# Kernel tuning notes

Hardware: AMD Instinct MI355X
Metric: run time of the kernel (lower is better)

## Reference

```python
import jax, jax.numpy as jnp
import numpy as np

FEAT = 128
N_RBF = 20
CUTOFF = 5.0
NUM_CONV = 3
N_ATOMS = 8000
N_EDGES = 160000
N_MOLS = 100
EPS = 1e-15


def silu(x):
    return x * jax.nn.sigmoid(x)


def setup_inputs() -> dict:
    key = jax.random.key(0)
    ks = jax.random.split(key, 16)
    F = FEAT

    def w(k, shape, fan_in):
        return jax.random.normal(k, shape, dtype=jnp.float32) / np.sqrt(fan_in).astype(np.float32)

    nbr0 = jax.random.randint(ks[12], (N_EDGES,), 0, N_ATOMS)
    # avoid self-edges (would give zero distance)
    nbr1 = (nbr0 + 1 + jax.random.randint(ks[13], (N_EDGES,), 0, N_ATOMS - 1)) % N_ATOMS
    return {
        "xyz": jax.random.uniform(ks[0], (N_ATOMS, 3), dtype=jnp.float32) * 10.0,
        "emb_table": jax.random.normal(ks[1], (100, F), dtype=jnp.float32),
        "msg_w1": w(ks[2], (NUM_CONV, F, F), F),
        "msg_b1": jnp.zeros((NUM_CONV, F), jnp.float32),
        "msg_w2": w(ks[3], (NUM_CONV, F, 3 * F), F),
        "msg_b2": jnp.zeros((NUM_CONV, 3 * F), jnp.float32),
        "rbf_w": w(ks[4], (NUM_CONV, N_RBF, 3 * F), N_RBF),
        "rbf_b": jnp.zeros((NUM_CONV, 3 * F), jnp.float32),
        "upd_u": w(ks[5], (NUM_CONV, F, F), F),
        "upd_v": w(ks[6], (NUM_CONV, F, F), F),
        "upd_w1": w(ks[7], (NUM_CONV, 2 * F, F), 2 * F),
        "upd_b1": jnp.zeros((NUM_CONV, F), jnp.float32),
        "upd_w2": w(ks[8], (NUM_CONV, F, 3 * F), F),
        "upd_b2": jnp.zeros((NUM_CONV, 3 * F), jnp.float32),
        "ro_w1": w(ks[9], (F, F // 2), F),
        "ro_b1": jnp.zeros((F // 2,), jnp.float32),
        "ro_w2": w(ks[10], (F // 2, 1), F // 2),
        "ro_b2": jnp.zeros((1,), jnp.float32),
        "z": jax.random.randint(ks[11], (N_ATOMS,), 0, 100),
        "nbrs": jnp.stack([nbr0, nbr1], axis=1),
        "mol_idx": jnp.sort(jax.random.randint(ks[14], (N_ATOMS,), 0, N_MOLS)),
    }


def painn_forward(xyz, emb_table, msg_w1, msg_b1, msg_w2, msg_b2, rbf_w, rbf_b,
                  upd_u, upd_v, upd_w1, upd_b1, upd_w2, upd_b2,
                  ro_w1, ro_b1, ro_w2, ro_b2, z, nbrs, mol_idx):
    F = FEAT
    N = xyz.shape[0]
    # r_ij points from nbrs[:,0] (center i) to nbrs[:,1] (neighbor j)
    r_ij = xyz[nbrs[:, 1]] - xyz[nbrs[:, 0]]            # (E, 3)
    d = jnp.sqrt(jnp.sum(r_ij * r_ij, axis=-1))         # (E,)
    unit = r_ij / d[:, None]                            # (E, 3)
    # PaiNN sinc radial basis: sin(n*pi*d/cutoff)/d, n = 1..n_rbf
    n = jnp.arange(1, N_RBF + 1, dtype=jnp.float32)
    rbf = jnp.sin(n[None, :] * jnp.pi * d[:, None] / CUTOFF) / d[:, None]  # (E, n_rbf)
    # cosine cutoff envelope
    env = jnp.where(d <= CUTOFF, 0.5 * (jnp.cos(jnp.pi * d / CUTOFF) + 1.0), 0.0)

    s = emb_table[z]                                    # (N, F)
    v = jnp.zeros((N, F, 3), dtype=s.dtype)             # (N, F, 3)

    for i in range(NUM_CONV):
        # ---- message block ----
        phi = silu(s @ msg_w1[i] + msg_b1[i]) @ msg_w2[i] + msg_b2[i]   # (N, 3F)
        w_s = (rbf @ rbf_w[i] + rbf_b[i]) * env[:, None]                # (E, 3F)
        inv = (phi[nbrs[:, 1]] * w_s).reshape(-1, 3, F)                 # (E, 3, F)
        split0 = inv[:, 0, :][..., None]                                # (E, F, 1)
        split1 = inv[:, 1, :]                                           # (E, F)
        split2 = inv[:, 2, :][..., None]                                # (E, F, 1)
        dv_ij = split2 * unit[:, None, :] + split0 * v[nbrs[:, 1]]      # (E, F, 3)
        ds = jax.ops.segment_sum(split1, nbrs[:, 0], num_segments=N)
        dv = jax.ops.segment_sum(dv_ij, nbrs[:, 0], num_segments=N)
        s = s + ds
        v = v + dv
        # ---- update block ----
        u_v = jnp.einsum('nfd,fg->ngd', v, upd_u[i])                    # (N, F, 3)
        v_v = jnp.einsum('nfd,fg->ngd', v, upd_v[i])                    # (N, F, 3)
        v_v_norm = jnp.sqrt(jnp.sum(v_v * v_v, axis=-1) + EPS)          # (N, F)
        stack = jnp.concatenate([s, v_v_norm], axis=-1)                 # (N, 2F)
        a = (silu(stack @ upd_w1[i] + upd_b1[i]) @ upd_w2[i] + upd_b2[i]).reshape(-1, 3, F)
        a_vv = a[:, 0, :][..., None]
        a_sv = a[:, 1, :]
        a_ss = a[:, 2, :]
        dv_u = u_v * a_vv
        ds_u = jnp.sum(u_v * v_v, axis=-1) * a_sv + a_ss
        s = s + ds_u
        v = v + dv_u

    # readout MLP + per-molecule sum pool (SumPool)
    atom_e = silu(s @ ro_w1 + ro_b1) @ ro_w2 + ro_b2                    # (N, 1)
    energy = jax.ops.segment_sum(atom_e, mol_idx, num_segments=N_MOLS)  # (N_MOLS, 1)
    return energy


def reference(xyz, emb_table, msg_w1, msg_b1, msg_w2, msg_b2, rbf_w, rbf_b,
              upd_u, upd_v, upd_w1, upd_b1, upd_w2, upd_b2,
              ro_w1, ro_b1, ro_w2, ro_b2, z, nbrs, mol_idx):
    return painn_forward(xyz, emb_table, msg_w1, msg_b1, msg_w2, msg_b2, rbf_w, rbf_b,
                         upd_u, upd_v, upd_w1, upd_b1, upd_w2, upd_b2,
                         ro_w1, ro_b1, ro_w2, ro_b2, z, nbrs, mol_idx)
```

## Files before the change

### kernel.cpp

```cpp
#include <hip/hip_runtime.h>

static constexpr int F = 128;
static constexpr int N_RBF = 20;
static constexpr int N_ATOMS = 8000;
static constexpr int NP = 8064;
static constexpr int N_EDGES = 160000;
static constexpr int N_MOLS = 100;
static constexpr float CUTOFF = 5.0f;
static constexpr size_t NFC = (size_t)NP * F;
static constexpr int REC = 28;
static constexpr int NPHI_BLK = NP / 32;
static constexpr int NBUILD_BLK = (N_EDGES + 255) / 256;
#define PIF 3.14159265358979323846f

typedef __attribute__((ext_vector_type(8))) short bf16x8;
typedef __attribute__((ext_vector_type(4))) float f32x4;
typedef unsigned short ushort_t;
typedef unsigned int uint_t;

__device__ __forceinline__ float silu_f(float x) { return x / (1.f + __expf(-x)); }

__device__ __forceinline__ ushort_t f2bf(float x) {
    union { float f; uint_t u; } v; v.f = x;
    uint_t r = v.u + 0x7fffu + ((v.u >> 16) & 1u);
// ... 220 lines not shown
                acc[i][j] = __builtin_amdgcn_mfma_f32_16x16x32_bf16(ahf[i], bhf[j], acc[i][j], 0, 0, 0);
                acc[i][j] = __builtin_amdgcn_mfma_f32_16x16x32_bf16(ahf[i], blf[j], acc[i][j], 0, 0, 0);
                acc[i][j] = __builtin_amdgcn_mfma_f32_16x16x32_bf16(alf[i], bhf[j], acc[i][j], 0, 0, 0);
            }
        if (it + 1 < 4) { writeA((it + 1) & 1); writeB((it + 1) & 1); }
        __syncthreads();
    }
    #pragma unroll
    for (int j = 0; j < 2; ++j) {
        int col = wn + j * 16 + row_l;
        float bval = b1[col];
        #pragma unroll
        for (int i = 0; i < 2; ++i)
            #pragma unroll
            for (int r = 0; r < 4; ++r) {
                int row = i * 16 + quad * 4 + r;
                float v = silu_f(acc[i][j][r] + bval);
                ushort_t h = f2bf(v);
                Hh[row * 136 + col] = h;
                Hl[row * 136 + col] = f2bf(v - bf2f(h));
            }
    }

    #pragma unroll
    for (int i = 0; i < 2; ++i)
        #pragma unroll
        for (int j = 0; j < 2; ++j)
            #pragma unroll
            for (int r = 0; r < 4; ++r) acc[i][j][r] = 0.f;
    loadB2(0); writeB(0);
    __syncthreads();
    #pragma unroll
    for (int it = 0; it < 12; ++it) {
        const int k0 = (it & 3) * 32;
        if (it + 1 < 12) loadB2(it + 1);
        bf16x8 ahf[2], alf[2], bhf[2], blf[2];
        #pragma unroll
        for (int i = 0; i < 2; ++i) {
            int ar = (i * 16 + row_l) * 136 + k0 + quad * 8;
            ahf[i] = *(const bf16x8*)&Hh[ar];
            alf[i] = *(const bf16x8*)&Hl[ar];
        }
        #pragma unroll
        for (int j = 0; j < 2; ++j) {
            int br = (wn + j * 16 + row_l) * 40 + quad * 8;
            bhf[j] = *(const bf16x8*)&Bh[it & 1][br];
            blf[j] = *(const bf16x8*)&Bl[it & 1][br];
        }
        #pragma unroll
        for (int i = 0; i < 2; ++i)
            #pragma unroll
            for (int j = 0; j < 2; ++j) {
                acc[i][j] = __builtin_amdgcn_mfma_f32_16x16x32_bf16(ahf[i], bhf[j], acc[i][j], 0, 0, 0);
                acc[i][j] = __builtin_amdgcn_mfma_f32_16x16x32_bf16(ahf[i], blf[j], acc[i][j], 0, 0, 0);
                acc[i][j] = __builtin_amdgcn_mfma_f32_16x16x32_bf16(alf[i], bhf[j], acc[i][j], 0, 0, 0);
            }
        if ((it & 3) == 3) {
            const int ct = it >> 2;
            #pragma unroll
            for (int j = 0; j < 2; ++j) {
                int col = ct * 128 + wn + j * 16 + row_l;
                float bval = b2[col];
                #pragma unroll
                for (int i = 0; i < 2; ++i)
                    #pragma unroll
                    for (int r = 0; r < 4; ++r) {
                        int row = i * 16 + quad * 4 + r;
                        C[(size_t)(m0 + row) * 384 + col] = acc[i][j][r] + bval;
                    }
            }
            #pragma unroll
            for (int i = 0; i < 2; ++i)
                #pragma unroll
                for (int j = 0; j < 2; ++j)
                    #pragma unroll
                    for (int r = 0; r < 4; ++r) acc[i][j][r] = 0.f;
        }
        if (it + 1 < 12) writeB((it + 1) & 1);
        __syncthreads();
    }
}

template<int TAIL>
__global__ __launch_bounds__(256) void updphi_kernel(
    float* __restrict__ s_io, float* __restrict__ v_io,
    const ushort_t* __restrict__ UVh, const ushort_t* __restrict__ UVl,
    const ushort_t* __restrict__ W1h, const ushort_t* __restrict__ W1l,
    const float* __restrict__ b1,
    const ushort_t* __restrict__ W2h, const ushort_t* __restrict__ W2l,
    const float* __restrict__ b2,
    const ushort_t* __restrict__ XW1h, const ushort_t* __restrict__ XW1l,
    const float* __restrict__ xb1,
    const ushort_t* __restrict__ XW2h, const ushort_t* __restrict__ XW2l,
    const float* __restrict__ xb2,
    float* __restrict__ phi_out,
    const float* __restrict__ w2ro, const float* __restrict__ b2ro,
    const int* __restrict__ mol, float* __restrict__ outp)
{
    __shared__ float uvv[96][260];
    __shared__ __align__(16) ushort_t Bh[2][128 * 40];
    __shared__ __align__(16) ushort_t Bl[2][128 * 40];
    __shared__ __align__(16) unsigned char AH[17408];
    __shared__ float molacc[128];
    __shared__ float redl[32][4];
    const int tid = threadIdx.x;
    const int wave = tid >> 6, lane = tid & 63;
    const int row_l = lane & 15, quad = lane >> 4;
    const int wn = wave * 32;
    const int m0 = blockIdx.x * 32;
    const int lrA = tid >> 3;
    const int ksA = (tid & 7) * 4;
    const int lrB = tid >> 1, ksB = (tid & 1) * 16;

    float* sS = &uvv[0][0];
    constexpr int SSTR = 132;

    {
        ushort_t* A0h = (ushort_t*)AH;
        ushort_t* A0l = A0h + 96 * 40;
        ushort_t* B0h = &Bh[0][0];
        ushort_t* B0l = &Bl[0][0];
        f32x4 acc0[6][4];
        #pragma unroll
        for (int i = 0; i < 6; ++i)
            #pragma unroll
            for (int j = 0; j < 4; ++j)
                #pragma unroll
                for (int r = 0; r < 4; ++r) acc0[i][j][r] = 0.f;
        for (int k0 = 0; k0 < 128; k0 += 32) {
            #pragma unroll
            for (int g = 0; g < 3; ++g) {
                int row = g * 32 + lrA;
                float4 v = *(const float4*)&v_io[(size_t)(m0 * 3 + row) * 128 + k0 + ksA];
                float e[4] = {v.x, v.y, v.z, v.w};
                ushort_t ph[4], pl[4];
                #pragma unroll
                for (int t = 0; t < 4; ++t) {
                    ushort_t h = f2bf(e[t]);
                    ph[t] = h; pl[t] = f2bf(e[t] - bf2f(h));
                }
                *(uint2*)&A0h[row * 40 + ksA] = *(uint2*)ph;
                *(uint2*)&A0l[row * 40 + ksA] = *(uint2*)pl;
            }
            {
                const ushort_t* bh = &UVh[(size_t)tid * 128 + k0];
                const ushort_t* bl = &UVl[(size_t)tid * 128 + k0];
                *(uint4*)&B0h[tid * 40 + 0]  = *(const uint4*)(bh + 0);
                *(uint4*)&B0h[tid * 40 + 8]  = *(const uint4*)(bh + 8);
                *(uint4*)&B0h[tid * 40 + 16] = *(const uint4*)(bh + 16);
                *(uint4*)&B0h[tid * 40 + 24] = *(const uint4*)(bh + 24);
                *(uint4*)&B0l[tid * 40 + 0]  = *(const uint4*)(bl + 0);
                *(uint4*)&B0l[tid * 40 + 8]  = *(const uint4*)(bl + 8);
                *(uint4*)&B0l[tid * 40 + 16] = *(const uint4*)(bl + 16);
                *(uint4*)&B0l[tid * 40 + 24] = *(const uint4*)(bl + 24);
            }
            __syncthreads();
            bf16x8 a0h[6], a0l[6], b0h[4], b0l[4];
            #pragma unroll
            for (int i = 0; i < 6; ++i) {
                int ar = (i * 16 + row_l) * 40 + quad * 8;
                a0h[i] = *(const bf16x8*)&A0h[ar];
                a0l[i] = *(const bf16x8*)&A0l[ar];
            }
            #pragma unroll
            for (int j = 0; j < 4; ++j) {
                int br = (wave * 64 + j * 16 + row_l) * 40 + quad * 8;
                b0h[j] = *(const bf16x8*)&B0h[br];
                b0l[j] = *(const bf16x8*)&B0l[br];
            }
            #pragma unroll
            for (int i = 0; i < 6; ++i)
                #pragma unroll
                for (int j = 0; j < 4; ++j) {
                    acc0[i][j] = __builtin_amdgcn_mfma_f32_16x16x32_bf16(a0h[i], b0h[j], acc0[i][j], 0, 0, 0);
                    acc0[i][j] = __builtin_amdgcn_mfma_f32_16x16x32_bf16(a0h[i], b0l[j], acc0[i][j], 0, 0, 0);
                    acc0[i][j] = __builtin_amdgcn_mfma_f32_16x16x32_bf16(a0l[i], b0h[j], acc0[i][j], 0, 0, 0);
                }
            __syncthreads();
        }
        #pragma unroll
        for (int i = 0; i < 6; ++i)
            #pragma unroll
            for (int j = 0; j < 4; ++j)
                #pragma unroll
                for (int r = 0; r < 4; ++r)
                    uvv[i * 16 + quad * 4 + r][wave * 64 + j * 16 + row_l] = acc0[i][j][r];
        __syncthreads();
    }

    ushort_t* Ah1 = (ushort_t*)AH;
    ushort_t* Al1 = Ah1 + 2 * 32 * 40;
    ushort_t* Hh  = (ushort_t*)AH;
    ushort_t* Hl  = Hh + 32 * 136;

    float4 rx;
    uint4 b_h0, b_h1, b_l0, b_l1;

    auto loadB1 = [&](int k0) {
        const ushort_t* bh = &W1h[(size_t)lrB * 256 + k0 + ksB];
        const ushort_t* bl = &W1l[(size_t)lrB * 256 + k0 + ksB];
        b_h0 = *(const uint4*)bh; b_h1 = *(const uint4*)(bh + 8);
        b_l0 = *(const uint4*)bl; b_l1 = *(const uint4*)(bl + 8);
    };
    auto writeB = [&](int buf) {
        *(uint4*)&Bh[buf][lrB * 40 + ksB]     = b_h0;
        *(uint4*)&Bh[buf][lrB * 40 + ksB + 8] = b_h1;
        *(uint4*)&Bl[buf][lrB * 40 + ksB]     = b_l0;
        *(uint4*)&Bl[buf][lrB * 40 + ksB + 8] = b_l1;
    };
    auto writeA1 = [&](int buf, int k0) {
        float e[4];
        if (k0 < 128) {
            e[0] = rx.x; e[1] = rx.y; e[2] = rx.z; e[3] = rx.w;
        } else {
            int f = k0 + ksA;
            #pragma unroll
            for (int t = 0; t < 4; ++t) {
                float x = uvv[lrA * 3 + 0][f + t];
                float y = uvv[lrA * 3 + 1][f + t];
                float z = uvv[lrA * 3 + 2][f + t];
                e[t] = sqrtf(x * x + y * y + z * z + 1e-15f);
            }
        }
        ushort_t ph[4], pl[4];
        #pragma unroll
        for (int t = 0; t < 4; ++t) {
            ushort_t h = f2bf(e[t]);
            ph[t] = h; pl[t] = f2bf(e[t] - bf2f(h));
        }
        *(uint2*)&Ah1[buf * 1280 + lrA * 40 + ksA] = *(uint2*)ph;
        *(uint2*)&Al1[buf * 1280 + lrA * 40 + ksA] = *(uint2*)pl;
    };

    f32x4 acc[2][2];
    #pragma unroll
    for (int i = 0; i < 2; ++i)
        #pragma unroll
        for (int j = 0; j < 2; ++j)
            #pragma unroll
            for (int r = 0; r < 4; ++r) acc[i][j][r] = 0.f;

    rx = *(const float4*)&s_io[(size_t)(m0 + lrA) * 128 + ksA];
    loadB1(0);
    writeA1(0, 0); writeB(0);
    __syncthreads();
    #pragma unroll
    for (int it = 0; it < 8; ++it) {
        const int k0n = (it + 1) * 32;
        if (it + 1 < 8) {
            if (k0n < 128) rx = *(const float4*)&s_io[(size_t)(m0 + lrA) * 128 + k0n + ksA];
            loadB1(k0n);
        }
        bf16x8 ahf[2], alf[2], bhf[2], blf[2];
        #pragma unroll
        for (int i = 0; i < 2; ++i) {
            int ar = (it & 1) * 1280 + (i * 16 + row_l) * 40 + quad * 8;
            ahf[i] = *(const bf16x8*)&Ah1[ar];
            alf[i] = *(const bf16x8*)&Al1[ar];
        }
        #pragma unroll
        for (int j = 0; j < 2; ++j) {
            int br = (wn + j * 16 + row_l) * 40 + quad * 8;
            bhf[j] = *(const bf16x8*)&Bh[it & 1][br];
            blf[j] = *(const bf16x8*)&Bl[it & 1][br];
        }
        #pragma unroll
        for (int i = 0; i < 2; ++i)
            #pragma unroll
            for (int j = 0; j < 2; ++j) {
                acc[i][j] = __builtin_amdgcn_mfma_f32_16x16x32_bf16(ahf[i], bhf[j], acc[i][j], 0, 0, 0);
                acc[i][j] = __builtin_amdgcn_mfma_f32_16x16x32_bf16(ahf[i], blf[j], acc[i][j], 0, 0, 0);
                acc[i][j] = __builtin_amdgcn_mfma_f32_16x16x32_bf16(alf[i], bhf[j], acc[i][j], 0, 0, 0);
            }
        if (it + 1 < 8) { writeA1((it + 1) & 1, k0n); writeB((it + 1) & 1); }
        __syncthreads();
    }
    #pragma unroll
    for (int j = 0; j < 2; ++j) {
        int col = wn + j * 16 + row_l;
        float bval = b1[col];
        #pragma unroll
        for (int i = 0; i < 2; ++i)
            #pragma unroll
            for (int r = 0; r < 4; ++r) {
                int row = i * 16 + quad * 4 + r;
                float v = silu_f(acc[i][j][r] + bval);
                ushort_t h = f2bf(v);
                Hh[row * 136 + col] = h;
                Hl[row * 136 + col] = f2bf(v - bf2f(h));
            }
    }

    constexpr int CT0 = TAIL ? 1 : 0;
    constexpr int NIT2 = (3 - CT0) * 4;
    auto loadB2 = [&](int it2) {
        int ct = CT0 + (it2 >> 2), k0 = (it2 & 3) * 32;
        const ushort_t* bh = &W2h[(size_t)(ct * 128 + lrB) * 128 + k0 + ksB];
        const ushort_t* bl = &W2l[(size_t)(ct * 128 + lrB) * 128 + k0 + ksB];
        b_h0 = *(const uint4*)bh; b_h1 = *(const uint4*)(bh + 8);
        b_l0 = *(const uint4*)bl; b_l1 = *(const uint4*)(bl + 8);
    };

    #pragma unroll
    for (int i = 0; i < 2; ++i)
        #pragma unroll
        for (int j = 0; j < 2; ++j)
            #pragma unroll
            for (int r = 0; r < 4; ++r) acc[i][j][r] = 0.f;
    f32x4 ssum[2][2];

    loadB2(0); writeB(0);
    __syncthreads();
    #pragma unroll
    for (int it = 0; it < NIT2; ++it) {
        const int k0 = (it & 3) * 32;
        if (it + 1 < NIT2) loadB2(it + 1);
        bf16x8 ahf[2], alf[2], bhf[2], blf[2];
        #pragma unroll
        for (int i = 0; i < 2; ++i) {
            int ar = (i * 16 + row_l) * 136 + k0 + quad * 8;
            ahf[i] = *(const bf16x8*)&Hh[ar];
            alf[i] = *(const bf16x8*)&Hl[ar];
        }
        #pragma unroll
        for (int j = 0; j < 2; ++j) {
            int br = (wn + j * 16 + row_l) * 40 + quad * 8;
            bhf[j] = *(const bf16x8*)&Bh[it & 1][br];
            blf[j] = *(const bf16x8*)&Bl[it & 1][br];
        }
        #pragma unroll
        for (int i = 0; i < 2; ++i)
            #pragma unroll
            for (int j = 0; j < 2; ++j) {
                acc[i][j] = __builtin_amdgcn_mfma_f32_16x16x32_bf16(ahf[i], bhf[j], acc[i][j], 0, 0, 0);
                acc[i][j] = __builtin_amdgcn_mfma_f32_16x16x32_bf16(ahf[i], blf[j], acc[i][j], 0, 0, 0);
                acc[i][j] = __builtin_amdgcn_mfma_f32_16x16x32_bf16(alf[i], bhf[j], acc[i][j], 0, 0, 0);
            }
        if ((it & 3) == 3) {
            const int ct = CT0 + (it >> 2);
            #pragma unroll
            for (int j = 0; j < 2; ++j) {
                int f = wn + j * 16 + row_l;
                float bval = b2[ct * 128 + f];
                #pragma unroll
                for (int i = 0; i < 2; ++i)
                    #pragma unroll
                    for (int r = 0; r < 4; ++r) {
                        int ln = i * 16 + quad * 4 + r;
                        float a = acc[i][j][r] + bval;
                        if (ct == 0) {
                            size_t vb = (size_t)(m0 + ln) * 3 * F + f;
                            v_io[vb]         += uvv[ln * 3 + 0][f] * a;
                            v_io[vb + F]     += uvv[ln * 3 + 1][f] * a;
                            v_io[vb + 2 * F] += uvv[ln * 3 + 2][f] * a;
                        } else if (ct == 1) {
                            float dot = uvv[ln * 3 + 0][f] * uvv[ln * 3 + 0][128 + f]
                                      + uvv[ln * 3 + 1][f] * uvv[ln * 3 + 1][128 + f]
                                      + uvv[ln * 3 + 2][f] * uvv[ln * 3 + 2][128 + f];
                            ssum[i][j][r] = dot * a;
                        } else {
                            float sv = s_io[(size_t)(m0 + ln) * F + f] + ssum[i][j][r] + a;
                            if constexpr (TAIL == 0) s_io[(size_t)(m0 + ln) * F + f] = sv;
                            sS[ln * SSTR + f] = sv;
                        }
                    }
            }
            #pragma unroll
            for (int i = 0; i < 2; ++i)
                #pragma unroll
                for (int j = 0; j < 2; ++j)
                    #pragma unroll
                    for (int r = 0; r < 4; ++r) acc[i][j][r] = 0.f;
        }
        if (it + 1 < NIT2) writeB((it + 1) & 1);
        __syncthreads();
    }

    if constexpr (TAIL == 1) { if (tid < 128) molacc[tid] = 0.f; }
    ushort_t* Ah3 = (ushort_t*)AH;
    ushort_t* Al3 = Ah3 + 2 * 1280;

    auto loadB31 = [&](int k0) {
        const ushort_t* bh = &XW1h[(size_t)lrB * 128 + k0 + ksB];
        const ushort_t* bl = &XW1l[(size_t)lrB * 128 + k0 + ksB];
        b_h0 = *(const uint4*)bh; b_h1 = *(const uint4*)(bh + 8);
        b_l0 = *(const uint4*)bl; b_l1 = *(const uint4*)(bl + 8);
    };
    auto writeA3 = [&](int buf, int k0) {
        float e[4];
        #pragma unroll
        for (int t = 0; t < 4; ++t) e[t] = sS[lrA * SSTR + k0 + ksA + t];
        ushort_t ph[4], pl[4];
        #pragma unroll
        for (int t = 0; t < 4; ++t) {
            ushort_t h = f2bf(e[t]);
            ph[t] = h; pl[t] = f2bf(e[t] - bf2f(h));
        }
        *(uint2*)&Ah3[buf * 1280 + lrA * 40 + ksA] = *(uint2*)ph;
        *(uint2*)&Al3[buf * 1280 + lrA * 40 + ksA] = *(uint2*)pl;
    };

    #pragma unroll
    for (int i = 0; i < 2; ++i)
        #pragma unroll
        for (int j = 0; j < 2; ++j)
            #pragma unroll
            for (int r = 0; r < 4; ++r) acc[i][j][r] = 0.f;

    loadB31(0);
    writeA3(0, 0); writeB(0);
    __syncthreads();
    #pragma unroll
    for (int it = 0; it < 4; ++it) {
        const int k0n = (it + 1) * 32;
        if (it + 1 < 4) loadB31(k0n);
        bf16x8 ahf[2], alf[2], bhf[2], blf[2];
        #pragma unroll
        for (int i = 0; i < 2; ++i) {
            int ar = (it & 1) * 1280 + (i * 16 + row_l) * 40 + quad * 8;
            ahf[i] = *(const bf16x8*)&Ah3[ar];
            alf[i] = *(const bf16x8*)&Al3[ar];
        }
        #pragma unroll
        for (int j = 0; j < 2; ++j) {
            int br = (wn + j * 16 + row_l) * 40 + quad * 8;
            bhf[j] = *(const bf16x8*)&Bh[it & 1][br];
            blf[j] = *(const bf16x8*)&Bl[it & 1][br];
        }
        #pragma unroll
        for (int i = 0; i < 2; ++i)
            #pragma unroll
            for (int j = 0; j < 2; ++j) {
                acc[i][j] = __builtin_amdgcn_mfma_f32_16x16x32_bf16(ahf[i], bhf[j], acc[i][j], 0, 0, 0);
                acc[i][j] = __builtin_amdgcn_mfma_f32_16x16x32_bf16(ahf[i], blf[j], acc[i][j], 0, 0, 0);
                acc[i][j] = __builtin_amdgcn_mfma_f32_16x16x32_bf16(alf[i], bhf[j], acc[i][j], 0, 0, 0);
            }
        if (it + 1 < 4) { writeA3((it + 1) & 1, k0n); writeB((it + 1) & 1); }
        __syncthreads();
    }

    if constexpr (TAIL == 0) {
        #pragma unroll
        for (int j = 0; j < 2; ++j) {
            int col = wn + j * 16 + row_l;
            float bval = xb1[col];
            #pragma unroll
            for (int i = 0; i < 2; ++i)
                #pragma unroll
                for (int r = 0; r < 4; ++r) {
                    int row = i * 16 + quad * 4 + r;
                    float v = silu_f(acc[i][j][r] + bval);
                    ushort_t h = f2bf(v);
                    Hh[row * 136 + col] = h;
                    Hl[row * 136 + col] = f2bf(v - bf2f(h));
                }
        }
        auto loadB32 = [&](int it2) {
            int ct = it2 >> 2, k0 = (it2 & 3) * 32;
            const ushort_t* bh = &XW2h[(size_t)(ct * 128 + lrB) * 128 + k0 + ksB];
            const ushort_t* bl = &XW2l[(size_t)(ct * 128 + lrB) * 128 + k0 + ksB];
            b_h0 = *(const uint4*)bh; b_h1 = *(const uint4*)(bh + 8);
            b_l0 = *(const uint4*)bl; b_l1 = *(const uint4*)(bl + 8);
        };
        #pragma unroll
        for (int i = 0; i < 2; ++i)
            #pragma unroll
            for (int j = 0; j < 2; ++j)
                #pragma unroll
                for (int r = 0; r < 4; ++r) acc[i][j][r] = 0.f;
        loadB32(0); writeB(0);
        __syncthreads();
        #pragma unroll
        for (int it = 0; it < 12; ++it) {
            const int k0 = (it & 3) * 32;
            if (it + 1 < 12) loadB32(it + 1);
            bf16x8 ahf[2], alf[2], bhf[2], blf[2];
            #pragma unroll
            for (int i = 0; i < 2; ++i) {
                int ar = (i * 16 + row_l) * 136 + k0 + quad * 8;
                ahf[i] = *(const bf16x8*)&Hh[ar];
                alf[i] = *(const bf16x8*)&Hl[ar];
            }
            #pragma unroll
            for (int j = 0; j < 2; ++j) {
                int br = (wn + j * 16 + row_l) * 40 + quad * 8;
                bhf[j] = *(const bf16x8*)&Bh[it & 1][br];
                blf[j] = *(const bf16x8*)&Bl[it & 1][br];
            }
            #pragma unroll
            for (int i = 0; i < 2; ++i)
                #pragma unroll
                for (int j = 0; j < 2; ++j) {
                    acc[i][j] = __builtin_amdgcn_mfma_f32_16x16x32_bf16(ahf[i], bhf[j], acc[i][j], 0, 0, 0);
                    acc[i][j] = __builtin_amdgcn_mfma_f32_16x16x32_bf16(ahf[i], blf[j], acc[i][j], 0, 0, 0);
                    acc[i][j] = __builtin_amdgcn_mfma_f32_16x16x32_bf16(alf[i], bhf[j], acc[i][j], 0, 0, 0);
                }
            if ((it & 3) == 3) {
                const int ct = it >> 2;
                #pragma unroll
                for (int j = 0; j < 2; ++j) {
                    int col = ct * 128 + wn + j * 16 + row_l;
                    float bval = xb2[col];
                    #pragma unroll
                    for (int i = 0; i < 2; ++i)
                        #pragma unroll
                        for (int r = 0; r < 4; ++r) {
                            int row = i * 16 + quad * 4 + r;
                            phi_out[(size_t)(m0 + row) * 384 + col] = acc[i][j][r] + bval;
                        }
                }
                #pragma unroll
                for (int i = 0; i < 2; ++i)
                    #pragma unroll
                    for (int j = 0; j < 2; ++j)
                        #pragma unroll
                        for (int r = 0; r < 4; ++r) acc[i][j][r] = 0.f;
            }
            if (it + 1 < 12) writeB((it + 1) & 1);
            __syncthreads();
        }
    } else {
        float part[2][4];
        #pragma unroll
        for (int i = 0; i < 2; ++i)
            #pragma unroll
            for (int r = 0; r < 4; ++r) part[i][r] = 0.f;
        #pragma unroll
        for (int j = 0; j < 2; ++j) {
            int col = wn + j * 16 + row_l;
            float bv = xb1[col];
            float wv = (col < 64) ? w2ro[col] : 0.f;
            #pragma unroll
            for (int i = 0; i < 2; ++i)
                #pragma unroll
                for (int r = 0; r < 4; ++r)
                    part[i][r] += silu_f(acc[i][j][r] + bv) * wv;
        }
        #pragma unroll
        for (int o = 1; o < 16; o <<= 1)
            #pragma unroll
            for (int i = 0; i < 2; ++i)
                #pragma unroll
                for (int r = 0; r < 4; ++r)
                    part[i][r] += __shfl_xor(part[i][r], o);
        if (row_l == 0)
            #pragma unroll
            for (int i = 0; i < 2; ++i)
                #pragma unroll
                for (int r = 0; r < 4; ++r)
                    redl[i * 16 + quad * 4 + r][wave] = part[i][r];
        __syncthreads();
        if (tid < 32) {
            int n = m0 + tid;
            if (n < N_ATOMS) {
                float e = redl[tid][0] + redl[tid][1] + redl[tid][2] + redl[tid][3] + b2ro[0];
                atomicAdd(&molacc[mol[n]], e);
            }
        }
        __syncthreads();
        if (tid < 100 && molacc[tid] != 0.f) atomicAdd(&outp[tid], molacc[tid]);
    }
}

template<int ZVIN>
__global__ __launch_bounds__(128) void msg_gather(
    const float* __restrict__ phi, const float* __restrict__ rec,
    const float* __restrict__ rbf_w, const float* __restrict__ rbf_b,
    const float* __restrict__ v_in, float* __restrict__ s,
    float* __restrict__ v_out, const int* __restrict__ offsets,
    const int* __restrict__ cnt)
{
    const int n = blockIdx.x, tid = threadIdx.x;
    float W0[N_RBF], W1[N_RBF], W2[N_RBF];
    #pragma unroll
    for (int k = 0; k < N_RBF; ++k) {
        W0[k] = rbf_w[k*3*F + tid];
        W1[k] = rbf_w[k*3*F + F + tid];
        W2[k] = rbf_w[k*3*F + 2*F + tid];
    }
    const float b0 = rbf_b[tid], b1 = rbf_b[F + tid], b2 = rbf_b[2*F + tid];
    float ds = 0.f, dvx = 0.f, dvy = 0.f, dvz = 0.f;
    const int off = offsets[n], c = cnt[n];
    const float* r = rec + (size_t)off * REC;
    #pragma unroll 2
    for (int t = 0; t < c; ++t, r += REC) {
        int j = __float_as_int(r[0]);
        float ev = r[1];
        float ux = r[2], uy = r[3], uz = r[4];
        float w0 = b0 * ev, w1 = b1 * ev, w2 = b2 * ev;
        #pragma unroll
        for (int k = 0; k < N_RBF; ++k) {
            float rk = r[5 + k];
            w0 += rk * W0[k]; w1 += rk * W1[k]; w2 += rk * W2[k];
        }
        const float* prow = phi + (size_t)j * 3 * F;
        float s0 = prow[tid] * w0;
        float s1 = prow[F + tid] * w1;
        float s2 = prow[2*F + tid] * w2;
        ds  += s1;
        if constexpr (ZVIN) {
            dvx += s2*ux; dvy += s2*uy; dvz += s2*uz;
        } else {
            const float* vrow = v_in + (size_t)j * 3 * F;
            dvx += s2*ux + s0 * vrow[tid];
            dvy += s2*uy + s0 * vrow[F + tid];
            dvz += s2*uz + s0 * vrow[2*F + tid];
        }
    }
    s[(size_t)n * F + tid] += ds;
    size_t vb = (size_t)n * 3 * F + tid;
    if constexpr (ZVIN) {
        v_out[vb]       = dvx;
        v_out[vb + F]   = dvy;
        v_out[vb + 2*F] = dvz;
    } else {
        v_out[vb]       = v_in[vb]       + dvx;
        v_out[vb + F]   = v_in[vb + F]   + dvy;
        v_out[vb + 2*F] = v_in[vb + 2*F] + dvz;
    }
}

extern "C" void kernel_launch(void* const* d_in, const int* in_sizes, int n_in,
                              void* d_out, int out_size, void* d_ws, size_t ws_size,
                              hipStream_t stream)
{
    const float* xyz    = (const float*)d_in[0];
    const float* emb    = (const float*)d_in[1];
    const float* msg_w1 = (const float*)d_in[2];
    const float* msg_b1 = (const float*)d_in[3];
    const float* msg_w2 = (const float*)d_in[4];
    const float* msg_b2 = (const float*)d_in[5];
    const float* rbf_w  = (const float*)d_in[6];
    const float* rbf_b  = (const float*)d_in[7];
    const float* upd_u  = (const float*)d_in[8];
    const float* upd_v  = (const float*)d_in[9];
    const float* upd_w1 = (const float*)d_in[10];
    const float* upd_b1 = (const float*)d_in[11];
    const float* upd_w2 = (const float*)d_in[12];
    const float* upd_b2 = (const float*)d_in[13];
    const float* ro_w1  = (const float*)d_in[14];
    const float* ro_b1  = (const float*)d_in[15];
    const float* ro_w2  = (const float*)d_in[16];
    const float* ro_b2  = (const float*)d_in[17];
    const int*   z      = (const int*)d_in[18];
    const int*   nbrs   = (const int*)d_in[19];
    const int*   molidx = (const int*)d_in[20];
    float* out = (float*)d_out;

    float* ws = (float*)d_ws;
    size_t off = 0;
    auto alloc = [&](size_t n) { float* p = ws + off; off += n; return p; };
    float* s_buf   = alloc(NFC);
    float* v1_buf  = alloc(3 * NFC);
    float* v2_buf  = alloc(3 * NFC);
    float* phi_buf = alloc(3 * NFC);
    float* envb    = alloc(N_EDGES);
    float* edgerec = alloc((size_t)N_EDGES * REC);
    ushort_t* wbf_hi = (ushort_t*)alloc(WPREP_W / 2 + 64);
    ushort_t* wbf_lo = (ushort_t*)alloc(WPREP_W / 2 + 64);
    float* robias   = alloc(128);
    int* cnt        = (int*)alloc(N_ATOMS);
    int* cursor     = (int*)alloc(N_ATOMS);
    int* offsets    = (int*)alloc(N_ATOMS);

    const size_t oW1 = 0, oW2 = 49152, oUV = 196608, oU1 = 294912, oU2 = 393216, oRO = 540672;

    prep_kernel<<<dim3(PREP_TOTAL / 256), dim3(256), 0, stream>>>(
        emb, z, s_buf,
        msg_w1, msg_w2, upd_u, upd_v, upd_w1, upd_w2, ro_w1, ro_b1,
        wbf_hi, wbf_lo, robias, cnt);
    count_kernel<<<dim3((N_EDGES + 255) / 256), dim3(256), 0, stream>>>(
        xyz, nbrs, envb, cnt);
    scan_kernel<<<dim3(1), dim3(1024), 0, stream>>>(cnt, offsets, out);
    build_phi0_kernel<<<dim3(NPHI_BLK + NBUILD_BLK), dim3(256), 0, stream>>>(
        xyz, nbrs, envb, offsets, cursor, edgerec,
        s_buf,
        wbf_hi + oW1, wbf_lo + oW1, msg_b1,
        wbf_hi + oW2, wbf_lo + oW2, msg_b2,
        phi_buf);

    float* vin = v1_buf;
    float* vout = v2_buf;
    for (int i = 0; i < 3; ++i) {
        if (i == 0)
            msg_gather<1><<<dim3(N_ATOMS), dim3(128), 0, stream>>>(
                phi_buf, edgerec, rbf_w + (size_t)i*N_RBF*3*F, rbf_b + (size_t)i*3*F,
                vin, s_buf, vout, offsets, cnt);
        else
            msg_gather<0><<<dim3(N_ATOMS), dim3(128), 0, stream>>>(
                phi_buf, edgerec, rbf_w + (size_t)i*N_RBF*3*F, rbf_b + (size_t)i*3*F,
                vin, s_buf, vout, offsets, cnt);
        if (i < 2) {
            updphi_kernel<0><<<dim3(NP/32), dim3(256), 0, stream>>>(
                s_buf, vout,
                wbf_hi + oUV + (size_t)i*32768, wbf_lo + oUV + (size_t)i*32768,
                wbf_hi + oU1 + (size_t)i*32768, wbf_lo + oU1 + (size_t)i*32768,
                upd_b1 + (size_t)i*F,
                wbf_hi + oU2 + (size_t)i*49152, wbf_lo + oU2 + (size_t)i*49152,
                upd_b2 + (size_t)i*3*F,
                wbf_hi + oW1 + (size_t)(i+1)*16384, wbf_lo + oW1 + (size_t)(i+1)*16384,
                msg_b1 + (size_t)(i+1)*F,
                wbf_hi + oW2 + (size_t)(i+1)*49152, wbf_lo + oW2 + (size_t)(i+1)*49152,
                msg_b2 + (size_t)(i+1)*3*F,
                phi_buf,
                nullptr, nullptr, nullptr, nullptr);
        } else {
            updphi_kernel<1><<<dim3(NP/32), dim3(256), 0, stream>>>(
                s_buf, vout,
                wbf_hi + oUV + (size_t)i*32768, wbf_lo + oUV + (size_t)i*32768,
                wbf_hi + oU1 + (size_t)i*32768, wbf_lo + oU1 + (size_t)i*32768,
                upd_b1 + (size_t)i*F,
                wbf_hi + oU2 + (size_t)i*49152, wbf_lo + oU2 + (size_t)i*49152,
                upd_b2 + (size_t)i*3*F,
                wbf_hi + oRO, wbf_lo + oRO, robias,
                nullptr, nullptr, nullptr,
                nullptr,
                ro_w2, ro_b2, molidx, out);
        }
        float* tmp = vin; vin = vout; vout = tmp;
    }
}
```

Before: 318.3 us.

## Double updphi block to 512 threads, splitting output columns across 8 waves

The fused update/phi kernel now runs 8 waves per 32-atom block instead of 4. Each wave owns 16 output columns instead of 32, and the UV GEMM uses 32 columns per wave. Staging loads are redistributed, with half the threads idle for A staging, and the readout reduction now sums 8 wave partials. This raises per-block parallelism and latency hiding at the cost of more barriers per unit of work, idle threads during A staging, and possibly lower occupancy from the larger block.

```diff
diff --git a/kernel.cpp b/kernel.cpp
--- a/kernel.cpp
+++ b/kernel.cpp
@@ -326,7 +326,7 @@
 }
 
 template<int TAIL>
-__global__ __launch_bounds__(256) void updphi_kernel(
+__global__ __launch_bounds__(512) void updphi_kernel(
     float* __restrict__ s_io, float* __restrict__ v_io,
     const ushort_t* __restrict__ UVh, const ushort_t* __restrict__ UVl,
     const ushort_t* __restrict__ W1h, const ushort_t* __restrict__ W1l,
@@ -346,15 +346,16 @@
     __shared__ __align__(16) ushort_t Bl[2][128 * 40];
     __shared__ __align__(16) unsigned char AH[17408];
     __shared__ float molacc[128];
-    __shared__ float redl[32][4];
+    __shared__ float redl[32][8];
     const int tid = threadIdx.x;
     const int wave = tid >> 6, lane = tid & 63;
     const int row_l = lane & 15, quad = lane >> 4;
-    const int wn = wave * 32;
+    const int wn16 = wave * 16;
+    const int wn32 = wave * 32;
     const int m0 = blockIdx.x * 32;
     const int lrA = tid >> 3;
     const int ksA = (tid & 7) * 4;
-    const int lrB = tid >> 1, ksB = (tid & 1) * 16;
+    const int lrB4 = tid >> 2, ksB4 = (tid & 3) * 8;
 
     float* sS = &uvv[0][0];
     constexpr int SSTR = 132;
@@ -364,42 +365,39 @@
         ushort_t* A0l = A0h + 96 * 40;
         ushort_t* B0h = &Bh[0][0];
         ushort_t* B0l = &Bl[0][0];
-        f32x4 acc0[6][4];
+        f32x4 acc0[6][2];
         #pragma unroll
         for (int i = 0; i < 6; ++i)
             #pragma unroll
-            for (int j = 0; j < 4; ++j)
+            for (int j = 0; j < 2; ++j)
                 #pragma unroll
                 for (int r = 0; r < 4; ++r) acc0[i][j][r] = 0.f;
+        auto stageA0 = [&](int row, int k0) {
+            float4 v = *(const float4*)&v_io[(size_t)(m0 * 3 + row) * 128 + k0 + ksA];
+            float e[4] = {v.x, v.y, v.z, v.w};
+            ushort_t ph[4], pl[4];
+            #pragma unroll
+            for (int t = 0; t < 4; ++t) {
+                ushort_t h = f2bf(e[t]);
+                ph[t] = h; pl[t] = f2bf(e[t] - bf2f(h));
+            }
+            *(uint2*)&A0h[row * 40 + ksA] = *(uint2*)ph;
+            *(uint2*)&A0l[row * 40 + ksA] = *(uint2*)pl;
+        };
         for (int k0 = 0; k0 < 128; k0 += 32) {
-            #pragma unroll
-            for (int g = 0; g < 3; ++g) {
-                int row = g * 32 + lrA;
-                float4 v = *(const float4*)&v_io[(size_t)(m0 * 3 + row) * 128 + k0 + ksA];
-                float e[4] = {v.x, v.y, v.z, v.w};
-                ushort_t ph[4], pl[4];
-                #pragma unroll
-                for (int t = 0; t < 4; ++t) {
-                    ushort_t h = f2bf(e[t]);
-                    ph[t] = h; pl[t] = f2bf(e[t] - bf2f(h));
-                }
-                *(uint2*)&A0h[row * 40 + ksA] = *(uint2*)ph;
-                *(uint2*)&A0l[row * 40 + ksA] = *(uint2*)pl;
-            }
+            stageA0(lrA, k0);
+            if (tid < 256) stageA0(64 + lrA, k0);
             {
-                const ushort_t* bh = &UVh[(size_t)tid * 128 + k0];
-                const ushort_t* bl = &UVl[(size_t)tid * 128 + k0];
-                *(uint4*)&B0h[tid * 40 + 0]  = *(const uint4*)(bh + 0);
-                *(uint4*)&B0h[tid * 40 + 8]  = *(const uint4*)(bh + 8);
-                *(uint4*)&B0h[tid * 40 + 16] = *(const uint4*)(bh + 16);
-                *(uint4*)&B0h[tid * 40 + 24] = *(const uint4*)(bh + 24);
-                *(uint4*)&B0l[tid * 40 + 0]  = *(const uint4*)(bl + 0);
-                *(uint4*)&B0l[tid * 40 + 8]  = *(const uint4*)(bl + 8);
-                *(uint4*)&B0l[tid * 40 + 16] = *(const uint4*)(bl + 16);
-                *(uint4*)&B0l[tid * 40 + 24] = *(const uint4*)(bl + 24);
+                int row = tid >> 1, hb = (tid & 1) * 16;
+                const ushort_t* bh = &UVh[(size_t)row * 128 + k0 + hb];
+                const ushort_t* bl = &UVl[(size_t)row * 128 + k0 + hb];
+                *(uint4*)&B0h[row * 40 + hb]     = *(const uint4*)bh;
+                *(uint4*)&B0h[row * 40 + hb + 8] = *(const uint4*)(bh + 8);
+                *(uint4*)&B0l[row * 40 + hb]     = *(const uint4*)bl;
+                *(uint4*)&B0l[row * 40 + hb + 8] = *(const uint4*)(bl + 8);
             }
             __syncthreads();
-            bf16x8 a0h[6], a0l[6], b0h[4], b0l[4];
+            bf16x8 a0h[6], a0l[6], b0h[2], b0l[2];
             #pragma unroll
             for (int i = 0; i < 6; ++i) {
                 int ar = (i * 16 + row_l) * 40 + quad * 8;
@@ -407,15 +405,15 @@
                 a0l[i] = *(const bf16x8*)&A0l[ar];
             }
             #pragma unroll
-            for (int j = 0; j < 4; ++j) {
-                int br = (wave * 64 + j * 16 + row_l) * 40 + quad * 8;
+            for (int j = 0; j < 2; ++j) {
+                int br = (wn32 + j * 16 + row_l) * 40 + quad * 8;
                 b0h[j] = *(const bf16x8*)&B0h[br];
                 b0l[j] = *(const bf16x8*)&B0l[br];
             }
             #pragma unroll
             for (int i = 0; i < 6; ++i)
                 #pragma unroll
-                for (int j = 0; j < 4; ++j) {
+                for (int j = 0; j < 2; ++j) {
                     acc0[i][j] = __builtin_amdgcn_mfma_f32_16x16x32_bf16(a0h[i], b0h[j], acc0[i][j], 0, 0, 0);
                     acc0[i][j] = __builtin_amdgcn_mfma_f32_16x16x32_bf16(a0h[i], b0l[j], acc0[i][j], 0, 0, 0);
                     acc0[i][j] = __builtin_amdgcn_mfma_f32_16x16x32_bf16(a0l[i], b0h[j], acc0[i][j], 0, 0, 0);
@@ -425,10 +423,10 @@
         #pragma unroll
         for (int i = 0; i < 6; ++i)
             #pragma unroll
-            for (int j = 0; j < 4; ++j)
+            for (int j = 0; j < 2; ++j)
                 #pragma unroll
                 for (int r = 0; r < 4; ++r)
-                    uvv[i * 16 + quad * 4 + r][wave * 64 + j * 16 + row_l] = acc0[i][j][r];
+                    uvv[i * 16 + quad * 4 + r][wn32 + j * 16 + row_l] = acc0[i][j][r];
         __syncthreads();
     }
 
@@ -438,19 +436,15 @@
     ushort_t* Hl  = Hh + 32 * 136;
 
     float4 rx;
-    uint4 b_h0, b_h1, b_l0, b_l1;
+    uint4 b_h0, b_l0;
 
     auto loadB1 = [&](int k0) {
-        const ushort_t* bh = &W1h[(size_t)lrB * 256 + k0 + ksB];
-        const ushort_t* bl = &W1l[(size_t)lrB * 256 + k0 + ksB];
-        b_h0 = *(const uint4*)bh; b_h1 = *(const uint4*)(bh + 8);
-        b_l0 = *(const uint4*)bl; b_l1 = *(const uint4*)(bl + 8);
+        b_h0 = *(const uint4*)&W1h[(size_t)lrB4 * 256 + k0 + ksB4];
+        b_l0 = *(const uint4*)&W1l[(size_t)lrB4 * 256 + k0 + ksB4];
     };
     auto writeB = [&](int buf) {
-        *(uint4*)&Bh[buf][lrB * 40 + ksB]     = b_h0;
-        *(uint4*)&Bh[buf][lrB * 40 + ksB + 8] = b_h1;
-        *(uint4*)&Bl[buf][lrB * 40 + ksB]     = b_l0;
-        *(uint4*)&Bl[buf][lrB * 40 + ksB + 8] = b_l1;
+        *(uint4*)&Bh[buf][lrB4 * 40 + ksB4] = b_h0;
+        *(uint4*)&Bl[buf][lrB4 * 40 + ksB4] = b_l0;
     };
     auto writeA1 = [&](int buf, int k0) {
         float e[4];
@@ -476,59 +470,54 @@
         *(uint2*)&Al1[buf * 1280 + lrA * 40 + ksA] = *(uint2*)pl;
     };
 
-    f32x4 acc[2][2];
+    f32x4 acc[2];
     #pragma unroll
     for (int i = 0; i < 2; ++i)
         #pragma unroll
-        for (int j = 0; j < 2; ++j)
-            #pragma unroll
-            for (int r = 0; r < 4; ++r) acc[i][j][r] = 0.f;
-
-    rx = *(const float4*)&s_io[(size_t)(m0 + lrA) * 128 + ksA];
+        for (int r = 0; r < 4; ++r) acc[i][r] = 0.f;
+
+    if (tid < 256) rx = *(const float4*)&s_io[(size_t)(m0 + lrA) * 128 + ksA];
     loadB1(0);
-    writeA1(0, 0); writeB(0);
+    if (tid < 256) writeA1(0, 0);
+    writeB(0);
     __syncthreads();
     #pragma unroll
     for (int it = 0; it < 8; ++it) {
         const int k0n = (it + 1) * 32;
         if (it + 1 < 8) {
-            if (k0n < 128) rx = *(const float4*)&s_io[(size_t)(m0 + lrA) * 128 + k0n + ksA];
+            if (tid < 256 && k0n < 128) rx = *(const float4*)&s_io[(size_t)(m0 + lrA) * 128 + k0n + ksA];
             loadB1(k0n);
         }
-        bf16x8 ahf[2], alf[2], bhf[2], blf[2];
+        bf16x8 ahf[2], alf[2], bhf, blf;
         #pragma unroll
         for (int i = 0; i < 2; ++i) {
             int ar = (it & 1) * 1280 + (i * 16 + row_l) * 40 + quad * 8;
             ahf[i] = *(const bf16x8*)&Ah1[ar];
             alf[i] = *(const bf16x8*)&Al1[ar];
         }
-        #pragma unroll
-        for (int j = 0; j < 2; ++j) {
-            int br = (wn + j * 16 + row_l) * 40 + quad * 8;
-            bhf[j] = *(const bf16x8*)&Bh[it & 1][br];
-            blf[j] = *(const bf16x8*)&Bl[it & 1][br];
-        }
-        #pragma unroll
-        for (int i = 0; i < 2; ++i)
-            #pragma unroll
-            for (int j = 0; j < 2; ++j) {
-                acc[i][j] = __builtin_amdgcn_mfma_f32_16x16x32_bf16(ahf[i], bhf[j], acc[i][j], 0, 0, 0);
-                acc[i][j] = __builtin_amdgcn_mfma_f32_16x16x32_bf16(ahf[i], blf[j], acc[i][j], 0, 0, 0);
-                acc[i][j] = __builtin_amdgcn_mfma_f32_16x16x32_bf16(alf[i], bhf[j], acc[i][j], 0, 0, 0);
-            }
-        if (it + 1 < 8) { writeA1((it + 1) & 1, k0n); writeB((it + 1) & 1); }
-        __syncthreads();
-    }
-    #pragma unroll
-    for (int j = 0; j < 2; ++j) {
-        int col = wn + j * 16 + row_l;
+        {
+            int br = (wn16 + row_l) * 40 + quad * 8;
+            bhf = *(const bf16x8*)&Bh[it & 1][br];
+            blf = *(const bf16x8*)&Bl[it & 1][br];
+        }
+        #pragma unroll
+        for (int i = 0; i < 2; ++i) {
+            acc[i] = __builtin_amdgcn_mfma_f32_16x16x32_bf16(ahf[i], bhf, acc[i], 0, 0, 0);
+            acc[i] = __builtin_amdgcn_mfma_f32_16x16x32_bf16(ahf[i], blf, acc[i], 0, 0, 0);
+            acc[i] = __builtin_amdgcn_mfma_f32_16x16x32_bf16(alf[i], bhf, acc[i], 0, 0, 0);
+        }
+        if (it + 1 < 8) { if (tid < 256) writeA1((it + 1) & 1, k0n); writeB((it + 1) & 1); }
+        __syncthreads();
+    }
+    {
+        int col = wn16 + row_l;
         float bval = b1[col];
         #pragma unroll
         for (int i = 0; i < 2; ++i)
             #pragma unroll
             for (int r = 0; r < 4; ++r) {
                 int row = i * 16 + quad * 4 + r;
-                float v = silu_f(acc[i][j][r] + bval);
+                float v = silu_f(acc[i][r] + bval);
                 ushort_t h = f2bf(v);
                 Hh[row * 136 + col] = h;
                 Hl[row * 136 + col] = f2bf(v - bf2f(h));
@@ -539,19 +528,15 @@
     constexpr int NIT2 = (3 - CT0) * 4;
     auto loadB2 = [&](int it2) {
         int ct = CT0 + (it2 >> 2), k0 = (it2 & 3) * 32;
-        const ushort_t* bh = &W2h[(size_t)(ct * 128 + lrB) * 128 + k0 + ksB];
-        const ushort_t* bl = &W2l[(size_t)(ct * 128 + lrB) * 128 + k0 + ksB];
-        b_h0 = *(const uint4*)bh; b_h1 = *(const uint4*)(bh + 8);
-        b_l0 = *(const uint4*)bl; b_l1 = *(const uint4*)(bl + 8);
+        b_h0 = *(const uint4*)&W2h[(size_t)(ct * 128 + lrB4) * 128 + k0 + ksB4];
+        b_l0 = *(const uint4*)&W2l[(size_t)(ct * 128 + lrB4) * 128 + k0 + ksB4];
     };
 
     #pragma unroll
     for (int i = 0; i < 2; ++i)
         #pragma unroll
-        for (int j = 0; j < 2; ++j)
-            #pragma unroll
-            for (int r = 0; r < 4; ++r) acc[i][j][r] = 0.f;
-    f32x4 ssum[2][2];
+        for (int r = 0; r < 4; ++r) acc[i][r] = 0.f;
+    f32x4 ssum[2];
 
     loadB2(0); writeB(0);
     __syncthreads();
@@ -559,62 +544,54 @@
     for (int it = 0; it < NIT2; ++it) {
         const int k0 = (it & 3) * 32;
         if (it + 1 < NIT2) loadB2(it + 1);
-        bf16x8 ahf[2], alf[2], bhf[2], blf[2];
+        bf16x8 ahf[2], alf[2], bhf, blf;
         #pragma unroll
         for (int i = 0; i < 2; ++i) {
             int ar = (i * 16 + row_l) * 136 + k0 + quad * 8;
             ahf[i] = *(const bf16x8*)&Hh[ar];
             alf[i] = *(const bf16x8*)&Hl[ar];
         }
-        #pragma unroll
-        for (int j = 0; j < 2; ++j) {
-            int br = (wn + j * 16 + row_l) * 40 + quad * 8;
-            bhf[j] = *(const bf16x8*)&Bh[it & 1][br];
-            blf[j] = *(const bf16x8*)&Bl[it & 1][br];
-        }
-        #pragma unroll
-        for (int i = 0; i < 2; ++i)
-            #pragma unroll
-            for (int j = 0; j < 2; ++j) {
-                acc[i][j] = __builtin_amdgcn_mfma_f32_16x16x32_bf16(ahf[i], bhf[j], acc[i][j], 0, 0, 0);
-                acc[i][j] = __builtin_amdgcn_mfma_f32_16x16x32_bf16(ahf[i], blf[j], acc[i][j], 0, 0, 0);
-                acc[i][j] = __builtin_amdgcn_mfma_f32_16x16x32_bf16(alf[i], bhf[j], acc[i][j], 0, 0, 0);
-            }
+        {
+            int br = (wn16 + row_l) * 40 + quad * 8;
+            bhf = *(const bf16x8*)&Bh[it & 1][br];
+            blf = *(const bf16x8*)&Bl[it & 1][br];
+        }
+        #pragma unroll
+        for (int i = 0; i < 2; ++i) {
+            acc[i] = __builtin_amdgcn_mfma_f32_16x16x32_bf16(ahf[i], bhf, acc[i], 0, 0, 0);
+            acc[i] = __builtin_amdgcn_mfma_f32_16x16x32_bf16(ahf[i], blf, acc[i], 0, 0, 0);
+            acc[i] = __builtin_amdgcn_mfma_f32_16x16x32_bf16(alf[i], bhf, acc[i], 0, 0, 0);
+        }
         if ((it & 3) == 3) {
             const int ct = CT0 + (it >> 2);
-            #pragma unroll
-            for (int j = 0; j < 2; ++j) {
-                int f = wn + j * 16 + row_l;
-                float bval = b2[ct * 128 + f];
-                #pragma unroll
-                for (int i = 0; i < 2; ++i)
-                    #pragma unroll
-                    for (int r = 0; r < 4; ++r) {
-                        int ln = i * 16 + quad * 4 + r;
-                        float a = acc[i][j][r] + bval;
-                        if (ct == 0) {
-                            size_t vb = (size_t)(m0 + ln) * 3 * F + f;
-                            v_io[vb]         += uvv[ln * 3 + 0][f] * a;
-                            v_io[vb + F]     += uvv[ln * 3 + 1][f] * a;
-                            v_io[vb + 2 * F] += uvv[ln * 3 + 2][f] * a;
-                        } else if (ct == 1) {
-                            float dot = uvv[ln * 3 + 0][f] * uvv[ln * 3 + 0][128 + f]
-                                      + uvv[ln * 3 + 1][f] * uvv[ln * 3 + 1][128 + f]
-                                      + uvv[ln * 3 + 2][f] * uvv[ln * 3 + 2][128 + f];
-                            ssum[i][j][r] = dot * a;
-                        } else {
-                            float sv = s_io[(size_t)(m0 + ln) * F + f] + ssum[i][j][r] + a;
-                            if constexpr (TAIL == 0) s_io[(size_t)(m0 + ln) * F + f] = sv;
-                            sS[ln * SSTR + f] = sv;
-                        }
+            int f = wn16 + row_l;
+            float bval = b2[ct * 128 + f];
+            #pragma unroll
+            for (int i = 0; i < 2; ++i)
+                #pragma unroll
+                for (int r = 0; r < 4; ++r) {
+                    int ln = i * 16 + quad * 4 + r;
+                    float a = acc[i][r] + bval;
+                    if (ct == 0) {
+                        size_t vb = (size_t)(m0 + ln) * 3 * F + f;
+                        v_io[vb]         += uvv[ln * 3 + 0][f] * a;
+                        v_io[vb + F]     += uvv[ln * 3 + 1][f] * a;
+                        v_io[vb + 2 * F] += uvv[ln * 3 + 2][f] * a;
+                    } else if (ct == 1) {
+                        float dot = uvv[ln * 3 + 0][f] * uvv[ln * 3 + 0][128 + f]
+                                  + uvv[ln * 3 + 1][f] * uvv[ln * 3 + 1][128 + f]
+                                  + uvv[ln * 3 + 2][f] * uvv[ln * 3 + 2][128 + f];
+                        ssum[i][r] = dot * a;
+                    } else {
+                        float sv = s_io[(size_t)(m0 + ln) * F + f] + ssum[i][r] + a;
+                        if constexpr (TAIL == 0) s_io[(size_t)(m0 + ln) * F + f] = sv;
+                        sS[ln * SSTR + f] = sv;
                     }
-            }
+                }
             #pragma unroll
             for (int i = 0; i < 2; ++i)
                 #pragma unroll
-                for (int j = 0; j < 2; ++j)
-                    #pragma unroll
-                    for (int r = 0; r < 4; ++r) acc[i][j][r] = 0.f;
+                for (int r = 0; r < 4; ++r) acc[i][r] = 0.f;
         }
         if (it + 1 < NIT2) writeB((it + 1) & 1);
         __syncthreads();
@@ -625,10 +602,8 @@
     ushort_t* Al3 = Ah3 + 2 * 1280;
 
     auto loadB31 = [&](int k0) {
-        const ushort_t* bh = &XW1h[(size_t)lrB * 128 + k0 + ksB];
-        const ushort_t* bl = &XW1l[(size_t)lrB * 128 + k0 + ksB];
-        b_h0 = *(const uint4*)bh; b_h1 = *(const uint4*)(bh + 8);
-        b_l0 = *(const uint4*)bl; b_l1 = *(const uint4*)(bl + 8);
+        b_h0 = *(const uint4*)&XW1h[(size_t)lrB4 * 128 + k0 + ksB4];
+        b_l0 = *(const uint4*)&XW1l[(size_t)lrB4 * 128 + k0 + ksB4];
     };
     auto writeA3 = [&](int buf, int k0) {
         float e[4];
@@ -647,53 +622,48 @@
     #pragma unroll
     for (int i = 0; i < 2; ++i)
         #pragma unroll
-        for (int j = 0; j < 2; ++j)
-            #pragma unroll
-            for (int r = 0; r < 4; ++r) acc[i][j][r] = 0.f;
+        for (int r = 0; r < 4; ++r) acc[i][r] = 0.f;
 
     loadB31(0);
-    writeA3(0, 0); writeB(0);
+    if (tid < 256) writeA3(0, 0);
+    writeB(0);
     __syncthreads();
     #pragma unroll
     for (int it = 0; it < 4; ++it) {
         const int k0n = (it + 1) * 32;
         if (it + 1 < 4) loadB31(k0n);
-        bf16x8 ahf[2], alf[2], bhf[2], blf[2];
+        bf16x8 ahf[2], alf[2], bhf, blf;
         #pragma unroll
         for (int i = 0; i < 2; ++i) {
             int ar = (it & 1) * 1280 + (i * 16 + row_l) * 40 + quad * 8;
             ahf[i] = *(const bf16x8*)&Ah3[ar];
             alf[i] = *(const bf16x8*)&Al3[ar];
         }
-        #pragma unroll
-        for (int j = 0; j < 2; ++j) {
-            int br = (wn + j * 16 + row_l) * 40 + quad * 8;
-            bhf[j] = *(const bf16x8*)&Bh[it & 1][br];
-            blf[j] = *(const bf16x8*)&Bl[it & 1][br];
-        }
-        #pragma unroll
-        for (int i = 0; i < 2; ++i)
-            #pragma unroll
-            for (int j = 0; j < 2; ++j) {
-                acc[i][j] = __builtin_amdgcn_mfma_f32_16x16x32_bf16(ahf[i], bhf[j], acc[i][j], 0, 0, 0);
-                acc[i][j] = __builtin_amdgcn_mfma_f32_16x16x32_bf16(ahf[i], blf[j], acc[i][j], 0, 0, 0);
-                acc[i][j] = __builtin_amdgcn_mfma_f32_16x16x32_bf16(alf[i], bhf[j], acc[i][j], 0, 0, 0);
-            }
-        if (it + 1 < 4) { writeA3((it + 1) & 1, k0n); writeB((it + 1) & 1); }
+        {
+            int br = (wn16 + row_l) * 40 + quad * 8;
+            bhf = *(const bf16x8*)&Bh[it & 1][br];
+            blf = *(const bf16x8*)&Bl[it & 1][br];
+        }
+        #pragma unroll
+        for (int i = 0; i < 2; ++i) {
+            acc[i] = __builtin_amdgcn_mfma_f32_16x16x32_bf16(ahf[i], bhf, acc[i], 0, 0, 0);
+            acc[i] = __builtin_amdgcn_mfma_f32_16x16x32_bf16(ahf[i], blf, acc[i], 0, 0, 0);
+            acc[i] = __builtin_amdgcn_mfma_f32_16x16x32_bf16(alf[i], bhf, acc[i], 0, 0, 0);
+        }
+        if (it + 1 < 4) { if (tid < 256) writeA3((it + 1) & 1, k0n); writeB((it + 1) & 1); }
         __syncthreads();
     }
 
     if constexpr (TAIL == 0) {
-        #pragma unroll
-        for (int j = 0; j < 2; ++j) {
-            int col = wn + j * 16 + row_l;
+        {
+            int col = wn16 + row_l;
             float bval = xb1[col];
             #pragma unroll
             for (int i = 0; i < 2; ++i)
                 #pragma unroll
                 for (int r = 0; r < 4; ++r) {
                     int row = i * 16 + quad * 4 + r;
-                    float v = silu_f(acc[i][j][r] + bval);
+                    float v = silu_f(acc[i][r] + bval);
                     ushort_t h = f2bf(v);
                     Hh[row * 136 + col] = h;
                     Hl[row * 136 + col] = f2bf(v - bf2f(h));
@@ -701,64 +671,52 @@
         }
         auto loadB32 = [&](int it2) {
             int ct = it2 >> 2, k0 = (it2 & 3) * 32;
-            const ushort_t* bh = &XW2h[(size_t)(ct * 128 + lrB) * 128 + k0 + ksB];
-            const ushort_t* bl = &XW2l[(size_t)(ct * 128 + lrB) * 128 + k0 + ksB];
-            b_h0 = *(const uint4*)bh; b_h1 = *(const uint4*)(bh + 8);
-            b_l0 = *(const uint4*)bl; b_l1 = *(const uint4*)(bl + 8);
+            b_h0 = *(const uint4*)&XW2h[(size_t)(ct * 128 + lrB4) * 128 + k0 + ksB4];
+            b_l0 = *(const uint4*)&XW2l[(size_t)(ct * 128 + lrB4) * 128 + k0 + ksB4];
         };
         #pragma unroll
         for (int i = 0; i < 2; ++i)
             #pragma unroll
-            for (int j = 0; j < 2; ++j)
-                #pragma unroll
-                for (int r = 0; r < 4; ++r) acc[i][j][r] = 0.f;
+            for (int r = 0; r < 4; ++r) acc[i][r] = 0.f;
         loadB32(0); writeB(0);
         __syncthreads();
         #pragma unroll
         for (int it = 0; it < 12; ++it) {
             const int k0 = (it & 3) * 32;
             if (it + 1 < 12) loadB32(it + 1);
-            bf16x8 ahf[2], alf[2], bhf[2], blf[2];
+            bf16x8 ahf[2], alf[2], bhf, blf;
             #pragma unroll
             for (int i = 0; i < 2; ++i) {
                 int ar = (i * 16 + row_l) * 136 + k0 + quad * 8;
                 ahf[i] = *(const bf16x8*)&Hh[ar];
                 alf[i] = *(const bf16x8*)&Hl[ar];
             }
-            #pragma unroll
-            for (int j = 0; j < 2; ++j) {
-                int br = (wn + j * 16 + row_l) * 40 + quad * 8;
-                bhf[j] = *(const bf16x8*)&Bh[it & 1][br];
-                blf[j] = *(const bf16x8*)&Bl[it & 1][br];
-            }
-            #pragma unroll
-            for (int i = 0; i < 2; ++i)
-                #pragma unroll
-                for (int j = 0; j < 2; ++j) {
-                    acc[i][j] = __builtin_amdgcn_mfma_f32_16x16x32_bf16(ahf[i], bhf[j], acc[i][j], 0, 0, 0);
-                    acc[i][j] = __builtin_amdgcn_mfma_f32_16x16x32_bf16(ahf[i], blf[j], acc[i][j], 0, 0, 0);
-                    acc[i][j] = __builtin_amdgcn_mfma_f32_16x16x32_bf16(alf[i], bhf[j], acc[i][j], 0, 0, 0);
-                }
+            {
+                int br = (wn16 + row_l) * 40 + quad * 8;
+                bhf = *(const bf16x8*)&Bh[it & 1][br];
+                blf = *(const bf16x8*)&Bl[it & 1][br];
+            }
+            #pragma unroll
+            for (int i = 0; i < 2; ++i) {
+                acc[i] = __builtin_amdgcn_mfma_f32_16x16x32_bf16(ahf[i], bhf, acc[i], 0, 0, 0);
+                acc[i] = __builtin_amdgcn_mfma_f32_16x16x32_bf16(ahf[i], blf, acc[i], 0, 0, 0);
+                acc[i] = __builtin_amdgcn_mfma_f32_16x16x32_bf16(alf[i], bhf, acc[i], 0, 0, 0);
+            }
             if ((it & 3) == 3) {
                 const int ct = it >> 2;
-                #pragma unroll
-                for (int j = 0; j < 2; ++j) {
-                    int col = ct * 128 + wn + j * 16 + row_l;
-                    float bval = xb2[col];
-                    #pragma unroll
-                    for (int i = 0; i < 2; ++i)
-                        #pragma unroll
-                        for (int r = 0; r < 4; ++r) {
-                            int row = i * 16 + quad * 4 + r;
-                            phi_out[(size_t)(m0 + row) * 384 + col] = acc[i][j][r] + bval;
-                        }
-                }
+                int col = ct * 128 + wn16 + row_l;
+                float bval = xb2[col];
                 #pragma unroll
                 for (int i = 0; i < 2; ++i)
                     #pragma unroll
-                    for (int j = 0; j < 2; ++j)
-                        #pragma unroll
-                        for (int r = 0; r < 4; ++r) acc[i][j][r] = 0.f;
+                    for (int r = 0; r < 4; ++r) {
+                        int row = i * 16 + quad * 4 + r;
+                        phi_out[(size_t)(m0 + row) * 384 + col] = acc[i][r] + bval;
+                    }
+                #pragma unroll
+                for (int i = 0; i < 2; ++i)
+                    #pragma unroll
+                    for (int r = 0; r < 4; ++r) acc[i][r] = 0.f;
             }
             if (it + 1 < 12) writeB((it + 1) & 1);
             __syncthreads();
@@ -769,16 +727,15 @@
         for (int i = 0; i < 2; ++i)
             #pragma unroll
             for (int r = 0; r < 4; ++r) part[i][r] = 0.f;
-        #pragma unroll
-        for (int j = 0; j < 2; ++j) {
-            int col = wn + j * 16 + row_l;
+        {
+            int col = wn16 + row_l;
             float bv = xb1[col];
             float wv = (col < 64) ? w2ro[col] : 0.f;
             #pragma unroll
             for (int i = 0; i < 2; ++i)
                 #pragma unroll
                 for (int r = 0; r < 4; ++r)
-                    part[i][r] += silu_f(acc[i][j][r] + bv) * wv;
+                    part[i][r] += silu_f(acc[i][r] + bv) * wv;
         }
         #pragma unroll
         for (int o = 1; o < 16; o <<= 1)
@@ -797,7 +754,8 @@
         if (tid < 32) {
             int n = m0 + tid;
             if (n < N_ATOMS) {
-                float e = redl[tid][0] + redl[tid][1] + redl[tid][2] + redl[tid][3] + b2ro[0];
+                float e = redl[tid][0] + redl[tid][1] + redl[tid][2] + redl[tid][3]
+                        + redl[tid][4] + redl[tid][5] + redl[tid][6] + redl[tid][7] + b2ro[0];
                 atomicAdd(&molacc[mol[n]], e);
             }
         }
@@ -935,7 +893,7 @@
                 phi_buf, edgerec, rbf_w + (size_t)i*N_RBF*3*F, rbf_b + (size_t)i*3*F,
                 vin, s_buf, vout, offsets, cnt);
         if (i < 2) {
-            updphi_kernel<0><<<dim3(NP/32), dim3(256), 0, stream>>>(
+            updphi_kernel<0><<<dim3(NP/32), dim3(512), 0, stream>>>(
                 s_buf, vout,
                 wbf_hi + oUV + (size_t)i*32768, wbf_lo + oUV + (size_t)i*32768,
                 wbf_hi + oU1 + (size_t)i*32768, wbf_lo + oU1 + (size_t)i*32768,
@@ -949,7 +907,7 @@
                 phi_buf,
                 nullptr, nullptr, nullptr, nullptr);
         } else {
-            updphi_kernel<1><<<dim3(NP/32), dim3(256), 0, stream>>>(
+            updphi_kernel<1><<<dim3(NP/32), dim3(512), 0, stream>>>(
                 s_buf, vout,
                 wbf_hi + oUV + (size_t)i*32768, wbf_lo + oUV + (size_t)i*32768,
                 wbf_hi + oU1 + (size_t)i*32768, wbf_lo + oU1 + (size_t)i*32768,
```

Measured after the change: 298.2 us. 6.3% less time.
